# Kernel tuning notes

Hardware: AMD Instinct MI355X
Metric: run time of the kernel (lower is better)

Reference implementation:

```python
import jax, jax.numpy as jnp
import numpy as np

B, T, D, H = 32, 2048, 512, 1024


def setup_inputs() -> dict:
    key = jax.random.key(0)
    ks = jax.random.split(key, 8)
    s = 1.0 / np.sqrt(H)  # torch nn.LSTM init scale
    x = jax.random.normal(ks[0], (B, T, D), jnp.float32)
    lengths = jnp.maximum(jax.random.randint(ks[1], (B,), 0, T), 1).astype(jnp.int32)
    h0 = jax.random.normal(ks[2], (1, B, H), jnp.float32)
    c0 = jax.random.normal(ks[3], (1, B, H), jnp.float32)
    W_ih = jax.random.uniform(ks[4], (4 * H, D), jnp.float32, -s, s)
    W_hh = jax.random.uniform(ks[5], (4 * H, H), jnp.float32, -s, s)
    b_ih = jax.random.uniform(ks[6], (4 * H,), jnp.float32, -s, s)
    b_hh = jax.random.uniform(ks[7], (4 * H,), jnp.float32, -s, s)
    return {"x": x, "lengths": lengths, "h0": h0, "c0": c0,
            "W_ih": W_ih, "W_hh": W_hh, "b_ih": b_ih, "b_hh": b_hh}


def _lstm_final(x, lengths, h0, c0, W_ih, W_hh, b_ih, b_hh):
    # Packed-sequence LSTM: final state per sequence == state at its last valid step.
    # Equivalent masked scan: freeze (h, c) once t >= length.
    t_len = x.shape[1]
    xt = jnp.swapaxes(x, 0, 1)                           # [T, B, D]
    mask = jnp.arange(t_len)[:, None] < lengths[None, :]  # [T, B]
    bias = b_ih + b_hh                                   # [4H]

    def step(carry, inp):
        h, c = carry                                     # [B, H] each
        xb, m = inp                                      # [B, D], [B]
        gates = xb @ W_ih.T + h @ W_hh.T + bias          # [B, 4H]
        i, f, g, o = jnp.split(gates, 4, axis=-1)        # torch gate order i,f,g,o
        c_new = jax.nn.sigmoid(f) * c + jax.nn.sigmoid(i) * jnp.tanh(g)
        h_new = jax.nn.sigmoid(o) * jnp.tanh(c_new)
        m = m[:, None]
        return (jnp.where(m, h_new, h), jnp.where(m, c_new, c)), None

    (h, c), _ = jax.lax.scan(step, (h0[0], c0[0]), (xt, mask))
    return h[None], c[None]                              # [1, B, H] each


def reference(x, lengths, h0, c0, W_ih, W_hh, b_ih, b_hh):
    return _lstm_final(x, lengths, h0, c0, W_ih, W_hh, b_ih, b_hh)
```

## Files before the change

### kernel.cpp

```cpp
#include <hip/hip_runtime.h>
#include <hip/hip_bf16.h>

#define B_ 32
#define T_ 2048
#define D_ 512
#define H_ 1024
#define G4_ 4096
#define NBLK 128
#define CG_ 64
#define JPB 16
#define MROW 16

typedef __attribute__((ext_vector_type(8))) short short8;
typedef __attribute__((ext_vector_type(4))) float f32x4;
typedef __attribute__((ext_vector_type(4))) int i32x4;

__device__ __forceinline__ float sigmoidf_(float x) { return 1.0f / (1.0f + __expf(-x)); }
__device__ __forceinline__ float tanhf_(float x) {
  float e = __expf(2.0f * x);
  return 1.0f - 2.0f / (e + 1.0f);
}
__device__ __forceinline__ unsigned short f_to_bf16bits(float f) {
  __hip_bfloat16 h = __float2bfloat16(f);
  return __builtin_bit_cast(unsigned short, h);
}

__device__ __forceinline__ i32x4 load16_sys(const void* p) {
  i32x4 v;
  asm volatile("global_load_dwordx4 %0, %1, off sc0 sc1" : "=v"(v) : "v"(p));
  return v;
}
__device__ __forceinline__ int load4_sys(const int* p) {
  int v;
  asm volatile("global_load_dword %0, %1, off sc0 sc1\n\t"
               "s_waitcnt vmcnt(0)"
               : "=v"(v) : "v"(p) : "memory");
  return v;
}
__device__ __forceinline__ void store16_sys(void* p, i32x4 v) {
  asm volatile("global_store_dwordx4 %0, %1, off sc0 sc1" :: "v"(p), "v"(v) : "memory");
}

__global__ __launch_bounds__(256) void xw_gemm(const float* __restrict__ x,
                                               const float* __restrict__ Wih,
                                               __hip_bfloat16* __restrict__ xg,
                                               int t0) {
  __shared__ __align__(16) __hip_bfloat16 As[128][40];
  __shared__ __align__(16) __hip_bfloat16 Bs[128][40];
  __shared__ __align__(16) __hip_bfloat16 Cs[128][132];

  const int tid = threadIdx.x;
  const int bx = blockIdx.x;
  const int by = blockIdx.y;
  const int lane = tid & 63, wave = tid >> 6;
  const int wm = wave >> 1, wn = wave & 1;
  const int lr = lane & 15, kq = (lane >> 4) * 8;

  const int r  = tid >> 1, ks = (tid & 1) * 16;
  const int rowA = by * 128 + r;
  const int bb = rowA & 31, tg = t0 + (rowA >> 5);
  const float* aptr = x  + ((size_t)bb * T_ + tg) * D_ + ks;
  const float* bptr = Wih + (size_t)(bx * 128 + r) * D_ + ks;

  f32x4 acc[4][4];
#pragma unroll
  for (int i = 0; i < 4; ++i)
#pragma unroll
    for (int jj = 0; jj < 4; ++jj) acc[i][jj] = (f32x4){0.f, 0.f, 0.f, 0.f};

  for (int k0 = 0; k0 < D_; k0 += 32) {
    __hip_bfloat16 ta[16], tb[16];
#pragma unroll
    for (int q = 0; q < 4; ++q) {
      f32x4 va = ((const f32x4*)(aptr + k0))[q];
      f32x4 vb = ((const f32x4*)(bptr + k0))[q];
#pragma unroll
      for (int e = 0; e < 4; ++e) {
        ta[q * 4 + e] = __float2bfloat16(va[e]);
        tb[q * 4 + e] = __float2bfloat16(vb[e]);
      }
    }
    __syncthreads();
    *(short8*)&As[r][ks]     = *(const short8*)&ta[0];
    *(short8*)&As[r][ks + 8] = *(const short8*)&ta[8];
    *(short8*)&Bs[r][ks]     = *(const short8*)&tb[0];
    *(short8*)&Bs[r][ks + 8] = *(const short8*)&tb[8];
    __syncthreads();

    short8 af[4], bf[4];
#pragma unroll
    for (int mi = 0; mi < 4; ++mi) af[mi] = *(const short8*)&As[wm * 64 + mi * 16 + lr][kq];
#pragma unroll
    for (int ni = 0; ni < 4; ++ni) bf[ni] = *(const short8*)&Bs[wn * 64 + ni * 16 + lr][kq];
#pragma unroll
    for (int mi = 0; mi < 4; ++mi)
#pragma unroll
      for (int ni = 0; ni < 4; ++ni)
        acc[mi][ni] = __builtin_amdgcn_mfma_f32_16x16x32_bf16(af[mi], bf[ni], acc[mi][ni], 0, 0, 0);
  }

#pragma unroll
  for (int mi = 0; mi < 4; ++mi)
#pragma unroll
    for (int ni = 0; ni < 4; ++ni)
#pragma unroll
      for (int rr = 0; rr < 4; ++rr)
        Cs[wm * 64 + mi * 16 + (lane >> 4) * 4 + rr][wn * 64 + ni * 16 + lr] =
            __float2bfloat16(acc[mi][ni][rr]);
  __syncthreads();

  const int orow = tid >> 1, oseg = (tid & 1) * 64;
  __hip_bfloat16* dst = xg + (size_t)(by * 128 + orow) * G4_ + bx * 128 + oseg;
#pragma unroll
  for (int c2 = 0; c2 < 8; ++c2)
    *(short8*)(dst + c2 * 8) = *(const short8*)&Cs[orow][oseg + c2 * 8];
}

__global__ __launch_bounds__(256, 1) void lstm_rec(
    const __hip_bfloat16* __restrict__ xg, const float* __restrict__ Whh,
    const int* __restrict__ lengths, const float* __restrict__ h0,
    const float* __restrict__ c0, const float* __restrict__ bih,
    const float* __restrict__ bhh, __hip_bfloat16* hbuf,
    float* __restrict__ hstate, float* __restrict__ cstate,
    int* flags, float* __restrict__ out,
    int t0, int t1, int isfirst, int islast) {
  __shared__ float Gs[4][MROW][68];

  const int bid = blockIdx.x, tid = threadIdx.x;
  const int bg = bid & 1, cg = bid >> 1;
  const int lane = tid & 63, w = tid >> 6;
  const int lr = lane & 15, q = lane >> 4, kq = q * 8;
  const int kkb = w * 8;

  short8 wf[4][8];
#pragma unroll
  for (int ni = 0; ni < 4; ++ni) {
    const int gcol = ni * H_ + cg * JPB + lr;
    const float* wbase = Whh + (size_t)gcol * H_ + kq;
#pragma unroll
    for (int kk2 = 0; kk2 < 8; ++kk2) {
      const int k0 = (kkb + kk2) * 32;
      f32x4 w0 = *(const f32x4*)(wbase + k0);
      f32x4 w1 = *(const f32x4*)(wbase + k0 + 4);
      __hip_bfloat16 tw_[8];
#pragma unroll
      for (int e = 0; e < 4; ++e) { tw_[e] = __float2bfloat16(w0[e]); tw_[4 + e] = __float2bfloat16(w1[e]); }
      wf[ni][kk2] = *(const short8*)&tw_[0];
    }
  }

  const int bloc = tid >> 4, j1 = tid & 15;
  const int b = bg * MROW + bloc;
  const int jglob = cg * JPB + j1;
  const int len_b = lengths[b];
  int maxlen = 0;
  for (int p = 0; p < B_; ++p) maxlen = max(maxlen, lengths[p]);
  const int tend = min(t1, maxlen);

  float hreg, creg, bias[4];
  if (isfirst) { hreg = h0[b * H_ + jglob]; creg = c0[b * H_ + jglob]; }
  else         { hreg = hstate[b * H_ + jglob]; creg = cstate[b * H_ + jglob]; }
#pragma unroll
  for (int p = 0; p < 4; ++p) bias[p] = bih[p * H_ + jglob] + bhh[p * H_ + jglob];

  const int* myflag = &flags[bg * CG_ + w * 16 + lr];
  char* const hstore_base = (char*)hbuf;
  const size_t poff = (size_t)b * (H_ * 2) + cg * (JPB * 2) + ((tid >> 3) & 1) * 16;

  for (int t = t0; t < tend; ++t) {
    float xv[4];
    {
      const __hip_bfloat16* xgrow = xg + ((size_t)(t - t0) * B_ + b) * G4_ + jglob;
#pragma unroll
      for (int p = 0; p < 4; ++p) xv[p] = __bfloat162float(xgrow[p * H_]);
    }

    while (true) {
      int f = load4_sys(myflag);
      if (__all((lane >= 16) || (f >= t))) break;
      __builtin_amdgcn_s_sleep(1);
    }

    const char* hb = (const char*)(hbuf + (size_t)(t & 1) * (B_ * H_));
    const char* rowp = hb + (size_t)(bg * MROW + lr) * (H_ * 2) + kkb * 64 + q * 16;
    i32x4 raw[8];
#pragma unroll
    for (int kk2 = 0; kk2 < 8; ++kk2)
      raw[kk2] = load16_sys(rowp + kk2 * 64);
    asm volatile("s_waitcnt vmcnt(0)" ::: "memory");
    __builtin_amdgcn_sched_barrier(0);

    short8 af[8];
#pragma unroll
    for (int kk2 = 0; kk2 < 8; ++kk2) {
      union { i32x4 i; short8 s; } cv;
      cv.i = raw[kk2];
      af[kk2] = cv.s;
    }

    f32x4 acc[4];
#pragma unroll
    for (int ni = 0; ni < 4; ++ni) acc[ni] = (f32x4){0.f, 0.f, 0.f, 0.f};
#pragma unroll
    for (int kk2 = 0; kk2 < 8; ++kk2)
#pragma unroll
      for (int ni = 0; ni < 4; ++ni)
        acc[ni] = __builtin_amdgcn_mfma_f32_16x16x32_bf16(af[kk2], wf[ni][kk2], acc[ni], 0, 0, 0);

#pragma unroll
    for (int ni = 0; ni < 4; ++ni)
#pragma unroll
      for (int rr = 0; rr < 4; ++rr)
        Gs[w][q * 4 + rr][ni * 16 + lr] = acc[ni][rr];
    __syncthreads();

    {
      const int upd = (t < len_b);
      float s[4];
#pragma unroll
      for (int p = 0; p < 4; ++p) {
        const int cb = p * 16 + j1;
        s[p] = (Gs[0][bloc][cb] + Gs[1][bloc][cb]) + (Gs[2][bloc][cb] + Gs[3][bloc][cb]);
      }
      const float ig = sigmoidf_(s[0] + xv[0] + bias[0]);
      const float fg = sigmoidf_(s[1] + xv[1] + bias[1]);
      const float gg = tanhf_(s[2] + xv[2] + bias[2]);
      const float og = sigmoidf_(s[3] + xv[3] + bias[3]);
      const float cn = fg * creg + ig * gg;
      const float hn = og * tanhf_(cn);
      if (upd) { creg = cn; hreg = hn; }

      unsigned int hb16 = (unsigned int)f_to_bf16bits(hreg);
      unsigned int a01 = (hb16 & 0xFFFFu) | (__shfl_xor(hb16, 1) << 16);
      unsigned int a23 = __shfl_xor(a01, 2);
      unsigned int a45 = __shfl_xor(a01, 4);
      unsigned int a67 = __shfl_xor(a23, 4);
      if ((tid & 7) == 0) {
        i32x4 v; v[0] = (int)a01; v[1] = (int)a23; v[2] = (int)a45; v[3] = (int)a67;
        store16_sys(hstore_base + (size_t)((t + 1) & 1) * (B_ * H_ * 2) + poff, v);
      }
      asm volatile("s_waitcnt vmcnt(0)" ::: "memory");
    }
    __syncthreads();
    if (tid == 0)
      __hip_atomic_store(&flags[bg * CG_ + cg], t + 1, __ATOMIC_RELAXED, __HIP_MEMORY_SCOPE_AGENT);
  }

  if (islast) {
    out[b * H_ + jglob] = hreg;
    out[B_ * H_ + b * H_ + jglob] = creg;
  } else {
    hstate[b * H_ + jglob] = hreg;
    cstate[b * H_ + jglob] = creg;
  }
}

__global__ void init_k(const float* __restrict__ h0, __hip_bfloat16* __restrict__ hbuf,
                       int* __restrict__ flags) {
  int i = blockIdx.x * 256 + threadIdx.x;
  if (i < B_ * H_) hbuf[i] = __float2bfloat16(h0[i]);
  if (i < NBLK) flags[i] = 0;
}

extern "C" void kernel_launch(void* const* d_in, const int* in_sizes, int n_in,
                              void* d_out, int out_size, void* d_ws, size_t ws_size,
                              hipStream_t stream) {
  const float* x       = (const float*)d_in[0];
  const int*   lengths = (const int*)d_in[1];
  const float* h0      = (const float*)d_in[2];
  const float* c0      = (const float*)d_in[3];
  const float* Wih     = (const float*)d_in[4];
  const float* Whh     = (const float*)d_in[5];
  const float* bih     = (const float*)d_in[6];
  const float* bhh     = (const float*)d_in[7];
  float* out = (float*)d_out;

  char* ws = (char*)d_ws;
  int* flags               = (int*)ws;
  __hip_bfloat16* hbuf     = (__hip_bfloat16*)(ws + 8192);
  float* hstate            = (float*)(ws + 8192 + 131072);
  float* cstate            = (float*)(ws + 8192 + 262144);
  __hip_bfloat16* xg       = (__hip_bfloat16*)(ws + 524288);

  size_t avail = (ws_size > 524288) ? ws_size - 524288 : 0;
  int tc = (int)(avail / ((size_t)B_ * G4_ * 2));
  if (tc > T_) tc = T_;
  tc &= ~3;
  if (tc < 4) tc = 4;

  hipLaunchKernelGGL(init_k, dim3(128), dim3(256), 0, stream, h0, hbuf, flags);
  for (int t0 = 0; t0 < T_; t0 += tc) {
    int len = min(tc, T_ - t0);
    dim3 gg(G4_ / 128, (len * B_) / 128);
    hipLaunchKernelGGL(xw_gemm, gg, dim3(256), 0, stream, x, Wih, xg, t0);
    hipLaunchKernelGGL(lstm_rec, dim3(NBLK), dim3(256), 0, stream,
                       xg, Whh, lengths, h0, c0, bih, bhh, hbuf, hstate, cstate,
                       flags, out, t0, t0 + len, (t0 == 0) ? 1 : 0,
                       (t0 + len >= T_) ? 1 : 0);
  }
}
```

Measured before the change: 9.244 ms.

## Fuse input projection into persistent LSTM recurrence kernel with register-resident W_ih

Drops the separate x·W_ih GEMM and its bf16 gate buffer in workspace. Each recurrent block now keeps its slice of W_ih in registers as bf16 MFMA fragments and computes the input contribution for each timestep before spinning on the flag. The aim is to remove the GEMM launches, the chunking over time and the round trip of the gate buffer through global memory, and to overlap the input MFMAs with waiting for h. The cost is higher register pressure and per-step fp32 loads of x inside the serial loop.

```diff
diff --git a/kernel.cpp b/kernel.cpp
--- a/kernel.cpp
+++ b/kernel.cpp
@@ -5,7 +5,6 @@
 #define T_ 2048
 #define D_ 512
 #define H_ 1024
-#define G4_ 4096
 #define NBLK 128
 #define CG_ 64
 #define JPB 16
@@ -41,89 +40,13 @@
   asm volatile("global_store_dwordx4 %0, %1, off sc0 sc1" :: "v"(p), "v"(v) : "memory");
 }
 
-__global__ __launch_bounds__(256) void xw_gemm(const float* __restrict__ x,
-                                               const float* __restrict__ Wih,
-                                               __hip_bfloat16* __restrict__ xg,
-                                               int t0) {
-  __shared__ __align__(16) __hip_bfloat16 As[128][40];
-  __shared__ __align__(16) __hip_bfloat16 Bs[128][40];
-  __shared__ __align__(16) __hip_bfloat16 Cs[128][132];
-
-  const int tid = threadIdx.x;
-  const int bx = blockIdx.x;
-  const int by = blockIdx.y;
-  const int lane = tid & 63, wave = tid >> 6;
-  const int wm = wave >> 1, wn = wave & 1;
-  const int lr = lane & 15, kq = (lane >> 4) * 8;
-
-  const int r  = tid >> 1, ks = (tid & 1) * 16;
-  const int rowA = by * 128 + r;
-  const int bb = rowA & 31, tg = t0 + (rowA >> 5);
-  const float* aptr = x  + ((size_t)bb * T_ + tg) * D_ + ks;
-  const float* bptr = Wih + (size_t)(bx * 128 + r) * D_ + ks;
-
-  f32x4 acc[4][4];
-#pragma unroll
-  for (int i = 0; i < 4; ++i)
-#pragma unroll
-    for (int jj = 0; jj < 4; ++jj) acc[i][jj] = (f32x4){0.f, 0.f, 0.f, 0.f};
-
-  for (int k0 = 0; k0 < D_; k0 += 32) {
-    __hip_bfloat16 ta[16], tb[16];
-#pragma unroll
-    for (int q = 0; q < 4; ++q) {
-      f32x4 va = ((const f32x4*)(aptr + k0))[q];
-      f32x4 vb = ((const f32x4*)(bptr + k0))[q];
-#pragma unroll
-      for (int e = 0; e < 4; ++e) {
-        ta[q * 4 + e] = __float2bfloat16(va[e]);
-        tb[q * 4 + e] = __float2bfloat16(vb[e]);
-      }
-    }
-    __syncthreads();
-    *(short8*)&As[r][ks]     = *(const short8*)&ta[0];
-    *(short8*)&As[r][ks + 8] = *(const short8*)&ta[8];
-    *(short8*)&Bs[r][ks]     = *(const short8*)&tb[0];
-    *(short8*)&Bs[r][ks + 8] = *(const short8*)&tb[8];
-    __syncthreads();
-
-    short8 af[4], bf[4];
-#pragma unroll
-    for (int mi = 0; mi < 4; ++mi) af[mi] = *(const short8*)&As[wm * 64 + mi * 16 + lr][kq];
-#pragma unroll
-    for (int ni = 0; ni < 4; ++ni) bf[ni] = *(const short8*)&Bs[wn * 64 + ni * 16 + lr][kq];
-#pragma unroll
-    for (int mi = 0; mi < 4; ++mi)
-#pragma unroll
-      for (int ni = 0; ni < 4; ++ni)
-        acc[mi][ni] = __builtin_amdgcn_mfma_f32_16x16x32_bf16(af[mi], bf[ni], acc[mi][ni], 0, 0, 0);
-  }
-
-#pragma unroll
-  for (int mi = 0; mi < 4; ++mi)
-#pragma unroll
-    for (int ni = 0; ni < 4; ++ni)
-#pragma unroll
-      for (int rr = 0; rr < 4; ++rr)
-        Cs[wm * 64 + mi * 16 + (lane >> 4) * 4 + rr][wn * 64 + ni * 16 + lr] =
-            __float2bfloat16(acc[mi][ni][rr]);
-  __syncthreads();
-
-  const int orow = tid >> 1, oseg = (tid & 1) * 64;
-  __hip_bfloat16* dst = xg + (size_t)(by * 128 + orow) * G4_ + bx * 128 + oseg;
-#pragma unroll
-  for (int c2 = 0; c2 < 8; ++c2)
-    *(short8*)(dst + c2 * 8) = *(const short8*)&Cs[orow][oseg + c2 * 8];
-}
-
 __global__ __launch_bounds__(256, 1) void lstm_rec(
-    const __hip_bfloat16* __restrict__ xg, const float* __restrict__ Whh,
+    const float* __restrict__ x, const float* __restrict__ Wih,
+    const float* __restrict__ Whh,
     const int* __restrict__ lengths, const float* __restrict__ h0,
     const float* __restrict__ c0, const float* __restrict__ bih,
     const float* __restrict__ bhh, __hip_bfloat16* hbuf,
-    float* __restrict__ hstate, float* __restrict__ cstate,
-    int* flags, float* __restrict__ out,
-    int t0, int t1, int isfirst, int islast) {
+    int* flags, float* __restrict__ out) {
   __shared__ float Gs[4][MROW][68];
 
   const int bid = blockIdx.x, tid = threadIdx.x;
@@ -146,6 +69,21 @@
 #pragma unroll
       for (int e = 0; e < 4; ++e) { tw_[e] = __float2bfloat16(w0[e]); tw_[4 + e] = __float2bfloat16(w1[e]); }
       wf[ni][kk2] = *(const short8*)&tw_[0];
+    }
+  }
+  short8 wfx[4][4];
+#pragma unroll
+  for (int ni = 0; ni < 4; ++ni) {
+    const int gcol = ni * H_ + cg * JPB + lr;
+    const float* wbase = Wih + (size_t)gcol * D_ + w * 128 + kq;
+#pragma unroll
+    for (int kkx = 0; kkx < 4; ++kkx) {
+      f32x4 w0 = *(const f32x4*)(wbase + kkx * 32);
+      f32x4 w1 = *(const f32x4*)(wbase + kkx * 32 + 4);
+      __hip_bfloat16 tw_[8];
+#pragma unroll
+      for (int e = 0; e < 4; ++e) { tw_[e] = __float2bfloat16(w0[e]); tw_[4 + e] = __float2bfloat16(w1[e]); }
+      wfx[ni][kkx] = *(const short8*)&tw_[0];
     }
   }
 
@@ -155,24 +93,39 @@
   const int len_b = lengths[b];
   int maxlen = 0;
   for (int p = 0; p < B_; ++p) maxlen = max(maxlen, lengths[p]);
-  const int tend = min(t1, maxlen);
-
-  float hreg, creg, bias[4];
-  if (isfirst) { hreg = h0[b * H_ + jglob]; creg = c0[b * H_ + jglob]; }
-  else         { hreg = hstate[b * H_ + jglob]; creg = cstate[b * H_ + jglob]; }
+  const int tend = maxlen;
+
+  float hreg = h0[b * H_ + jglob], creg = c0[b * H_ + jglob];
+  float bias[4];
 #pragma unroll
   for (int p = 0; p < 4; ++p) bias[p] = bih[p * H_ + jglob] + bhh[p * H_ + jglob];
 
   const int* myflag = &flags[bg * CG_ + w * 16 + lr];
   char* const hstore_base = (char*)hbuf;
   const size_t poff = (size_t)b * (H_ * 2) + cg * (JPB * 2) + ((tid >> 3) & 1) * 16;
-
-  for (int t = t0; t < tend; ++t) {
-    float xv[4];
+  const float* xrow = x + (size_t)(bg * MROW + lr) * T_ * D_ + w * 128 + kq;
+
+  for (int t = 0; t < tend; ++t) {
+    f32x4 acc[4];
+#pragma unroll
+    for (int ni = 0; ni < 4; ++ni) acc[ni] = (f32x4){0.f, 0.f, 0.f, 0.f};
     {
-      const __hip_bfloat16* xgrow = xg + ((size_t)(t - t0) * B_ + b) * G4_ + jglob;
-#pragma unroll
-      for (int p = 0; p < 4; ++p) xv[p] = __bfloat162float(xgrow[p * H_]);
+      const float* xt = xrow + (size_t)t * D_;
+      short8 afx[4];
+#pragma unroll
+      for (int kkx = 0; kkx < 4; ++kkx) {
+        f32x4 a0 = *(const f32x4*)(xt + kkx * 32);
+        f32x4 a1 = *(const f32x4*)(xt + kkx * 32 + 4);
+        __hip_bfloat16 ta_[8];
+#pragma unroll
+        for (int e = 0; e < 4; ++e) { ta_[e] = __float2bfloat16(a0[e]); ta_[4 + e] = __float2bfloat16(a1[e]); }
+        afx[kkx] = *(const short8*)&ta_[0];
+      }
+#pragma unroll
+      for (int kkx = 0; kkx < 4; ++kkx)
+#pragma unroll
+        for (int ni = 0; ni < 4; ++ni)
+          acc[ni] = __builtin_amdgcn_mfma_f32_16x16x32_bf16(afx[kkx], wfx[ni][kkx], acc[ni], 0, 0, 0);
     }
 
     while (true) {
@@ -198,9 +151,6 @@
       af[kk2] = cv.s;
     }
 
-    f32x4 acc[4];
-#pragma unroll
-    for (int ni = 0; ni < 4; ++ni) acc[ni] = (f32x4){0.f, 0.f, 0.f, 0.f};
 #pragma unroll
     for (int kk2 = 0; kk2 < 8; ++kk2)
 #pragma unroll
@@ -222,10 +172,10 @@
         const int cb = p * 16 + j1;
         s[p] = (Gs[0][bloc][cb] + Gs[1][bloc][cb]) + (Gs[2][bloc][cb] + Gs[3][bloc][cb]);
       }
-      const float ig = sigmoidf_(s[0] + xv[0] + bias[0]);
-      const float fg = sigmoidf_(s[1] + xv[1] + bias[1]);
-      const float gg = tanhf_(s[2] + xv[2] + bias[2]);
-      const float og = sigmoidf_(s[3] + xv[3] + bias[3]);
+      const float ig = sigmoidf_(s[0] + bias[0]);
+      const float fg = sigmoidf_(s[1] + bias[1]);
+      const float gg = tanhf_(s[2] + bias[2]);
+      const float og = sigmoidf_(s[3] + bias[3]);
       const float cn = fg * creg + ig * gg;
       const float hn = og * tanhf_(cn);
       if (upd) { creg = cn; hreg = hn; }
@@ -246,13 +196,8 @@
       __hip_atomic_store(&flags[bg * CG_ + cg], t + 1, __ATOMIC_RELAXED, __HIP_MEMORY_SCOPE_AGENT);
   }
 
-  if (islast) {
-    out[b * H_ + jglob] = hreg;
-    out[B_ * H_ + b * H_ + jglob] = creg;
-  } else {
-    hstate[b * H_ + jglob] = hreg;
-    cstate[b * H_ + jglob] = creg;
-  }
+  out[b * H_ + jglob] = hreg;
+  out[B_ * H_ + b * H_ + jglob] = creg;
 }
 
 __global__ void init_k(const float* __restrict__ h0, __hip_bfloat16* __restrict__ hbuf,
@@ -278,24 +223,8 @@
   char* ws = (char*)d_ws;
   int* flags               = (int*)ws;
   __hip_bfloat16* hbuf     = (__hip_bfloat16*)(ws + 8192);
-  float* hstate            = (float*)(ws + 8192 + 131072);
-  float* cstate            = (float*)(ws + 8192 + 262144);
-  __hip_bfloat16* xg       = (__hip_bfloat16*)(ws + 524288);
-
-  size_t avail = (ws_size > 524288) ? ws_size - 524288 : 0;
-  int tc = (int)(avail / ((size_t)B_ * G4_ * 2));
-  if (tc > T_) tc = T_;
-  tc &= ~3;
-  if (tc < 4) tc = 4;
 
   hipLaunchKernelGGL(init_k, dim3(128), dim3(256), 0, stream, h0, hbuf, flags);
-  for (int t0 = 0; t0 < T_; t0 += tc) {
-    int len = min(tc, T_ - t0);
-    dim3 gg(G4_ / 128, (len * B_) / 128);
-    hipLaunchKernelGGL(xw_gemm, gg, dim3(256), 0, stream, x, Wih, xg, t0);
-    hipLaunchKernelGGL(lstm_rec, dim3(NBLK), dim3(256), 0, stream,
-                       xg, Whh, lengths, h0, c0, bih, bhh, hbuf, hstate, cstate,
-                       flags, out, t0, t0 + len, (t0 == 0) ? 1 : 0,
-                       (t0 + len >= T_) ? 1 : 0);
-  }
-}
+  hipLaunchKernelGGL(lstm_rec, dim3(NBLK), dim3(256), 0, stream,
+                     x, Wih, Whh, lengths, h0, c0, bih, bhh, hbuf, flags, out);
+}
```

Measured after the change: 8.033 ms. 1.15x faster.
